# Optimization experiments

Measured on AMD Instinct MI355X. Metric: run time of the kernel, lower is better.

The kernel has to match this reference:

```python
import jax, jax.numpy as jnp
import numpy as np

DIM = 32  # fixed internal node dim
N_GRAPHS = 64


def setup_inputs() -> dict:
    key = jax.random.key(0)
    ks = jax.random.split(key, 16)
    N, E, F_N, F_E, H = 12500, 200000, 16, 8, 32
    inp = {
        "x": jax.random.normal(ks[0], (N, F_N), dtype=jnp.float32),
        "edge_index": jax.random.randint(ks[1], (2, E), 0, N, dtype=jnp.int64),
        "edge_attr": jax.random.normal(ks[2], (E, F_E), dtype=jnp.float32),
        "batch": jnp.sort(jax.random.randint(ks[3], (N,), 0, N_GRAPHS, dtype=jnp.int64)),
        "lin0_w": jax.random.normal(ks[4], (DIM, F_N), dtype=jnp.float32) * 0.1,
        "lin0_b": jax.random.normal(ks[5], (DIM,), dtype=jnp.float32) * 0.1,
        "nn_w": jax.random.normal(ks[6], (DIM * H, F_E), dtype=jnp.float32) * 0.1,
        "nn_b": jax.random.normal(ks[7], (DIM * H,), dtype=jnp.float32) * 0.1,
        "root_w": jax.random.normal(ks[8], (DIM, H), dtype=jnp.float32) * 0.1,
        "conv_b": jax.random.normal(ks[9], (H,), dtype=jnp.float32) * 0.1,
        "lin1_w": jax.random.normal(ks[10], (16, H), dtype=jnp.float32) * 0.1,
        "lin1_b": jax.random.normal(ks[11], (16,), dtype=jnp.float32) * 0.1,
        "lin2_w": jax.random.normal(ks[12], (1, 16), dtype=jnp.float32) * 0.1,
        "lin2_b": jax.random.normal(ks[13], (1,), dtype=jnp.float32) * 0.1,
    }
    return inp


def reference(x, edge_index, edge_attr, batch, lin0_w, lin0_b, nn_w, nn_b,
              root_w, conv_b, lin1_w, lin1_b, lin2_w, lin2_b):
    N = x.shape[0]
    H = conv_b.shape[0]
    # lin0 + relu -> node features [N, DIM]
    out = jax.nn.relu(x @ lin0_w.T + lin0_b)
    # NNConv: per-edge weight matrices from edge MLP (single Linear)
    src, dst = edge_index[0], edge_index[1]
    w_e = (edge_attr @ nn_w.T + nn_b).reshape(-1, DIM, H)  # [E, DIM, H]
    msg = jnp.einsum('ed,edh->eh', out[src], w_e)          # gather + per-edge matmul
    agg = jax.ops.segment_sum(msg, dst, num_segments=N)     # scatter-add
    h = jax.nn.relu(agg + out @ root_w + conv_b)             # root weight + bias
    # global add pool over graphs
    u = jax.ops.segment_sum(h, batch, num_segments=N_GRAPHS)  # [G, H]
    o = jax.nn.relu(u @ lin1_w.T + lin1_b)
    o = o @ lin2_w.T + lin2_b
    return o.reshape(-1)
```

## Files before the change

### kernel.cpp

```cpp
#include <hip/hip_runtime.h>

#define DIMN 32
#define HD   32
#define FN   16
#define FE   8
#define NG   64
#define CAP  64
#define K3T  512
#define K3W  (K3T / 64)

__global__ __launch_bounds__(256) void k1_out(
    const float* __restrict__ x, const float* __restrict__ lin0_w,
    const float* __restrict__ lin0_b,
    float* __restrict__ outn, float* __restrict__ aggfb, float* __restrict__ u,
    int* __restrict__ deg, int N)
{
    const int gt = blockIdx.x * 256 + threadIdx.x;
    if (gt >= N * DIMN) return;
    const int n = gt >> 5, d = gt & 31;

    float s = lin0_b[d];
    const float* xr = x + (size_t)n * FN;
    const float* wr = lin0_w + d * FN;
    #pragma unroll
    for (int j = 0; j < FN; ++j) s = fmaf(xr[j], wr[j], s);
    outn[gt] = fmaxf(s, 0.f);

    aggfb[gt] = 0.f;
    if (d == 0) deg[n] = 0;
    if (gt < NG * HD) u[gt] = 0.f;
}

__global__ __launch_bounds__(256) void kb_bucket(
    const int* __restrict__ ei, const float* __restrict__ ea,
    const float* __restrict__ outn, const float* __restrict__ nn_w,
    const float* __restrict__ nn_b,
    int* __restrict__ deg, int2* __restrict__ es, float* __restrict__ aggfb, int E)
{
    const int e = blockIdx.x * 256 + threadIdx.x;
    if (e >= E) return;
    const int src = ei[e];
    const int dst = ei[E + e];
    const int pos = atomicAdd(&deg[dst], 1);
    if (pos < CAP) {
        es[(size_t)dst * CAP + pos] = make_int2(e, src);
    } else {
        float ef[FE];
        #pragma unroll
        for (int f = 0; f < FE; ++f) ef[f] = ea[(size_t)e * FE + f];
        for (int h = 0; h < HD; ++h) {
            float m = 0.f;
            for (int d = 0; d < DIMN; ++d) {
                float wdh = nn_b[d * HD + h];
                #pragma unroll
                for (int f = 0; f < FE; ++f)
                    wdh = fmaf(ef[f], nn_w[(d * HD + h) * FE + f], wdh);
                m = fmaf(outn[(size_t)src * DIMN + d], wdh, m);
            }
            atomicAdd(aggfb + (size_t)dst * HD + h, m);
        }
    }
}

#define EDGE_FMA(o, a) \
    S  = (S + (o));                      \
    T0 = fmaf((o), (a).x, T0);           \
    T1 = fmaf((o), (a).y, T1);           \
    T2 = fmaf((o), (a).z, T2);           \
    T3 = fmaf((o), (a).w, T3);

#define CONTRIB(DD, A) { \
    const int d_ = d0 + (DD); \
    const float4 ta_ = *(const float4*)&s_T[w * 256 + d_ * 8]; \
    const float4 tb_ = *(const float4*)&s_T[w * 256 + d_ * 8 + 4]; \
    const float2 so_ = s_SO[w * 32 + d_]; \
    const int b_ = d_ * 256 + h; \
    A = fmaf(ta_.x, s_nnw2[b_      ], A); \
    A = fmaf(ta_.y, s_nnw2[b_ +  32], A); \
    A = fmaf(ta_.z, s_nnw2[b_ +  64], A); \
    A = fmaf(ta_.w, s_nnw2[b_ +  96], A); \
    A = fmaf(tb_.x, s_nnw2[b_ + 128], A); \
    A = fmaf(tb_.y, s_nnw2[b_ + 160], A); \
    A = fmaf(tb_.z, s_nnw2[b_ + 192], A); \
    A = fmaf(tb_.w, s_nnw2[b_ + 224], A); \
    A = fmaf(so_.x, s_nnb[d_ * 32 + h], A); \
    A = fmaf(so_.y, s_rw [d_ * 32 + h], A); }

__global__ __launch_bounds__(K3T, 8) void k3_gather(
    const float* __restrict__ ea, const float* __restrict__ outn,
    const int2* __restrict__ es, const float* __restrict__ nn_w,
    const float* __restrict__ nn_b, const float* __restrict__ root_w,
    const float* __restrict__ conv_b, const int* __restrict__ deg,
    const float* __restrict__ aggfb, const int* __restrict__ batch,
    float* __restrict__ u, int N)
{
    __shared__ float  s_nnw2[DIMN * FE * HD];
    __shared__ float  s_nnb[DIMN * HD];
    __shared__ float  s_rw[DIMN * HD];
    __shared__ float  s_cb[HD];
    __shared__ float  s_T[K3W * 256];
    __shared__ float2 s_SO[K3W * 32];
    __shared__ float  s_V[K3W * 32];
    __shared__ int    s_G[K3W];

    const int tid = threadIdx.x;
    for (int i = tid; i < DIMN * FE * HD; i += K3T) {
        const int d = i >> 8, rem = i & 255, hh = rem >> 3, f = rem & 7;
        s_nnw2[(d * 8 + f) * 32 + hh] = nn_w[i];
    }
    for (int i = tid; i < DIMN * HD; i += K3T) { s_nnb[i] = nn_b[i]; s_rw[i] = root_w[i]; }
    if (tid < HD) s_cb[tid] = conv_b[tid];
    __syncthreads();

    const int l = tid & 63;
    const int h = l & 31;
    const int p = l >> 5;
    const int w = tid >> 6;
    const int n = blockIdx.x * K3W + w;

    int gval = -1;
    if (n < N) {
        const int nu = __builtin_amdgcn_readfirstlane(n);
        const int dn = min(deg[nu], CAP);
        const int2* ep = es + (size_t)nu * CAP;
        const int f0 = 4 * p;

        float T0 = 0.f, T1 = 0.f, T2 = 0.f, T3 = 0.f, S = 0.f;

        for (int j0 = 0; j0 < dn; j0 += 8) {
            const int jm = dn - 1;
            const int2 E0 = ep[j0];
            const int2 E1 = ep[min(j0 + 1, jm)];
            const int2 E2 = ep[min(j0 + 2, jm)];
            const int2 E3 = ep[min(j0 + 3, jm)];
            const int2 E4 = ep[min(j0 + 4, jm)];
            const int2 E5 = ep[min(j0 + 5, jm)];
            const int2 E6 = ep[min(j0 + 6, jm)];
            const int2 E7 = ep[min(j0 + 7, jm)];

            const float4 a0 = *(const float4*)(ea + (size_t)E0.x * FE + f0);
            const float4 a1 = *(const float4*)(ea + (size_t)E1.x * FE + f0);
            const float4 a2 = *(const float4*)(ea + (size_t)E2.x * FE + f0);
            const float4 a3 = *(const float4*)(ea + (size_t)E3.x * FE + f0);
            const float4 a4 = *(const float4*)(ea + (size_t)E4.x * FE + f0);
            const float4 a5 = *(const float4*)(ea + (size_t)E5.x * FE + f0);
            const float4 a6 = *(const float4*)(ea + (size_t)E6.x * FE + f0);
            const float4 a7 = *(const float4*)(ea + (size_t)E7.x * FE + f0);
            float o0 = outn[(size_t)E0.y * DIMN + h];
            float o1 = outn[(size_t)E1.y * DIMN + h];
            float o2 = outn[(size_t)E2.y * DIMN + h];
            float o3 = outn[(size_t)E3.y * DIMN + h];
            float o4 = outn[(size_t)E4.y * DIMN + h];
            float o5 = outn[(size_t)E5.y * DIMN + h];
            float o6 = outn[(size_t)E6.y * DIMN + h];
            float o7 = outn[(size_t)E7.y * DIMN + h];

            o1 = (j0 + 1 <= jm) ? o1 : 0.f;
            o2 = (j0 + 2 <= jm) ? o2 : 0.f;
            o3 = (j0 + 3 <= jm) ? o3 : 0.f;
            o4 = (j0 + 4 <= jm) ? o4 : 0.f;
            o5 = (j0 + 5 <= jm) ? o5 : 0.f;
            o6 = (j0 + 6 <= jm) ? o6 : 0.f;
            o7 = (j0 + 7 <= jm) ? o7 : 0.f;

            EDGE_FMA(o0, a0) EDGE_FMA(o1, a1) EDGE_FMA(o2, a2) EDGE_FMA(o3, a3)
            EDGE_FMA(o4, a4) EDGE_FMA(o5, a5) EDGE_FMA(o6, a6) EDGE_FMA(o7, a7)
        }

        *(float4*)&s_T[w * 256 + h * 8 + f0] = make_float4(T0, T1, T2, T3);
        if (p == 0) s_SO[w * 32 + h] = make_float2(S, outn[(size_t)nu * DIMN + h]);

        const float base = aggfb[(size_t)nu * HD + h] + s_cb[h];

        float acc0 = 0.f, acc1 = 0.f, acc2 = 0.f, acc3 = 0.f;
        const int d0 = p << 4;
        #pragma unroll
        for (int dd = 0; dd < 16; dd += 4) {
            CONTRIB(dd + 0, acc0)
            CONTRIB(dd + 1, acc1)
            CONTRIB(dd + 2, acc2)
            CONTRIB(dd + 3, acc3)
        }
        float acc = (acc0 + acc1) + (acc2 + acc3);
        acc += __shfl_xor(acc, 32);

        const float v = fmaxf(acc + base, 0.f);
        if (p == 0) s_V[w * 32 + h] = v;
        gval = batch[nu];
    }
    if (l == 0) s_G[w] = gval;
    __syncthreads();

    if (tid < 32) {
        float accp = 0.f;
        int   gc   = -1;
        #pragma unroll
        for (int ww = 0; ww < K3W; ++ww) {
            const int gg = s_G[ww];
            if (gg >= 0) {
                const float vv = s_V[ww * 32 + tid];
                if (gg != gc) {
                    if (gc >= 0) atomicAdd(u + (size_t)gc * HD + tid, accp);
                    gc = gg;
                    accp = vv;
                } else {
                    accp += vv;
                }
            }
        }
        if (gc >= 0) atomicAdd(u + (size_t)gc * HD + tid, accp);
    }
}

__global__ __launch_bounds__(64) void k4_head(
    const float* __restrict__ u, const float* __restrict__ lin1_w,
    const float* __restrict__ lin1_b, const float* __restrict__ lin2_w,
    const float* __restrict__ lin2_b, float* __restrict__ outp)
{
    const int g = threadIdx.x;
    if (g >= NG) return;

    float ur[HD];
    #pragma unroll
    for (int hh = 0; hh < HD; ++hh) ur[hh] = u[(size_t)g * HD + hh];

    float acc = lin2_b[0];
    #pragma unroll
    for (int i = 0; i < 16; ++i) {
        float o = lin1_b[i];
        #pragma unroll
        for (int hh = 0; hh < HD; ++hh)
            o = fmaf(ur[hh], lin1_w[i * HD + hh], o);
        o = fmaxf(o, 0.f);
        acc = fmaf(o, lin2_w[i], acc);
    }
    outp[g] = acc;
}

extern "C" void kernel_launch(void* const* d_in, const int* in_sizes, int n_in,
                              void* d_out, int out_size, void* d_ws, size_t ws_size,
                              hipStream_t stream)
{
    const float* x      = (const float*)d_in[0];
    const int*   ei     = (const int*)  d_in[1];
    const float* ea     = (const float*)d_in[2];
    const int*   batch  = (const int*)  d_in[3];
    const float* lin0_w = (const float*)d_in[4];
    const float* lin0_b = (const float*)d_in[5];
    const float* nn_w   = (const float*)d_in[6];
    const float* nn_b   = (const float*)d_in[7];
    const float* root_w = (const float*)d_in[8];
    const float* conv_b = (const float*)d_in[9];
    const float* lin1_w = (const float*)d_in[10];
    const float* lin1_b = (const float*)d_in[11];
    const float* lin2_w = (const float*)d_in[12];
    const float* lin2_b = (const float*)d_in[13];

    const int N = in_sizes[0] / FN;
    const int E = in_sizes[2] / FE;

    float* ws    = (float*)d_ws;
    float* outn  = ws;
    float* aggfb = outn  + (size_t)N * DIMN;
    float* u     = aggfb + (size_t)N * DIMN;
    int*   deg   = (int*)(u + (size_t)NG * HD);
    int2*  es    = (int2*)(deg + N);

    const int nb1 = (N * DIMN + 255) / 256;
    k1_out<<<nb1, 256, 0, stream>>>(x, lin0_w, lin0_b, outn, aggfb, u, deg, N);

    const int nbb = (E + 255) / 256;
    kb_bucket<<<nbb, 256, 0, stream>>>(ei, ea, outn, nn_w, nn_b, deg, es, aggfb, E);

    const int nb3 = (N + K3W - 1) / K3W;
    k3_gather<<<nb3, K3T, 0, stream>>>(ea, outn, es, nn_w, nn_b, root_w, conv_b,
                                       deg, aggfb, batch, u, N);

    k4_head<<<1, 64, 0, stream>>>(u, lin1_w, lin1_b, lin2_w, lin2_b, (float*)d_out);
}
```

Baseline: 141.7 us.

## Process two destination nodes per wavefront in gather kernel with interleaved edge loops

Each wavefront in the gather kernel now handles two consecutive destination nodes. It interleaves their edge loads four edges at a time, so more independent gathers are in flight per iteration. The block count is halved and the occupancy hint is lowered from 8 to 6 to make room for the extra accumulator registers. The first bucket slot of every node is zero-initialised so clamped indices stay safe when a node has no edges. The trade-off is lower occupancy and wasted lanes whenever the two nodes' degrees differ.

```diff
diff --git a/kernel.cpp b/kernel.cpp
--- a/kernel.cpp
+++ b/kernel.cpp
@@ -8,12 +8,13 @@
 #define CAP  64
 #define K3T  512
 #define K3W  (K3T / 64)
+#define K3NPB (K3W * 2)
 
 __global__ __launch_bounds__(256) void k1_out(
     const float* __restrict__ x, const float* __restrict__ lin0_w,
     const float* __restrict__ lin0_b,
     float* __restrict__ outn, float* __restrict__ aggfb, float* __restrict__ u,
-    int* __restrict__ deg, int N)
+    int* __restrict__ deg, int2* __restrict__ es, int N)
 {
     const int gt = blockIdx.x * 256 + threadIdx.x;
     if (gt >= N * DIMN) return;
@@ -27,7 +28,7 @@
     outn[gt] = fmaxf(s, 0.f);
 
     aggfb[gt] = 0.f;
-    if (d == 0) deg[n] = 0;
+    if (d == 0) { deg[n] = 0; es[(size_t)n * CAP] = make_int2(0, 0); }
     if (gt < NG * HD) u[gt] = 0.f;
 }
 
@@ -62,12 +63,14 @@
     }
 }
 
-#define EDGE_FMA(o, a) \
-    S  = (S + (o));                      \
-    T0 = fmaf((o), (a).x, T0);           \
-    T1 = fmaf((o), (a).y, T1);           \
-    T2 = fmaf((o), (a).z, T2);           \
-    T3 = fmaf((o), (a).w, T3);
+#define EDGE_FMA_A(o, a) \
+    SA += (o); \
+    TA0 = fmaf((o), (a).x, TA0);  TA1 = fmaf((o), (a).y, TA1); \
+    TA2 = fmaf((o), (a).z, TA2);  TA3 = fmaf((o), (a).w, TA3);
+#define EDGE_FMA_B(o, a) \
+    SB += (o); \
+    TB0 = fmaf((o), (a).x, TB0);  TB1 = fmaf((o), (a).y, TB1); \
+    TB2 = fmaf((o), (a).z, TB2);  TB3 = fmaf((o), (a).w, TB3);
 
 #define CONTRIB(DD, A) { \
     const int d_ = d0 + (DD); \
@@ -86,7 +89,7 @@
     A = fmaf(so_.x, s_nnb[d_ * 32 + h], A); \
     A = fmaf(so_.y, s_rw [d_ * 32 + h], A); }
 
-__global__ __launch_bounds__(K3T, 8) void k3_gather(
+__global__ __launch_bounds__(K3T, 6) void k3_gather(
     const float* __restrict__ ea, const float* __restrict__ outn,
     const int2* __restrict__ es, const float* __restrict__ nn_w,
     const float* __restrict__ nn_b, const float* __restrict__ root_w,
@@ -100,8 +103,8 @@
     __shared__ float  s_cb[HD];
     __shared__ float  s_T[K3W * 256];
     __shared__ float2 s_SO[K3W * 32];
-    __shared__ float  s_V[K3W * 32];
-    __shared__ int    s_G[K3W];
+    __shared__ float  s_V[K3NPB * 32];
+    __shared__ int    s_G[K3NPB];
 
     const int tid = threadIdx.x;
     for (int i = tid; i < DIMN * FE * HD; i += K3T) {
@@ -116,86 +119,115 @@
     const int h = l & 31;
     const int p = l >> 5;
     const int w = tid >> 6;
-    const int n = blockIdx.x * K3W + w;
-
-    int gval = -1;
-    if (n < N) {
-        const int nu = __builtin_amdgcn_readfirstlane(n);
-        const int dn = min(deg[nu], CAP);
-        const int2* ep = es + (size_t)nu * CAP;
+    const int nA = blockIdx.x * K3NPB + 2 * w;
+
+    int gA = -1, gB = -1;
+    if (nA < N) {
+        const int nuA = __builtin_amdgcn_readfirstlane(nA);
+        const bool vB = (nuA + 1) < N;
+        const int nuB = vB ? nuA + 1 : nuA;
+        const int dnA = min(deg[nuA], CAP);
+        const int dnB = vB ? min(deg[nuB], CAP) : 0;
+        const int2* epA = es + (size_t)nuA * CAP;
+        const int2* epB = es + (size_t)nuB * CAP;
+        const int jmA = max(dnA - 1, 0);
+        const int jmB = max(dnB - 1, 0);
+        const int dmax = max(dnA, dnB);
         const int f0 = 4 * p;
 
-        float T0 = 0.f, T1 = 0.f, T2 = 0.f, T3 = 0.f, S = 0.f;
-
-        for (int j0 = 0; j0 < dn; j0 += 8) {
-            const int jm = dn - 1;
-            const int2 E0 = ep[j0];
-            const int2 E1 = ep[min(j0 + 1, jm)];
-            const int2 E2 = ep[min(j0 + 2, jm)];
-            const int2 E3 = ep[min(j0 + 3, jm)];
-            const int2 E4 = ep[min(j0 + 4, jm)];
-            const int2 E5 = ep[min(j0 + 5, jm)];
-            const int2 E6 = ep[min(j0 + 6, jm)];
-            const int2 E7 = ep[min(j0 + 7, jm)];
-
-            const float4 a0 = *(const float4*)(ea + (size_t)E0.x * FE + f0);
-            const float4 a1 = *(const float4*)(ea + (size_t)E1.x * FE + f0);
-            const float4 a2 = *(const float4*)(ea + (size_t)E2.x * FE + f0);
-            const float4 a3 = *(const float4*)(ea + (size_t)E3.x * FE + f0);
-            const float4 a4 = *(const float4*)(ea + (size_t)E4.x * FE + f0);
-            const float4 a5 = *(const float4*)(ea + (size_t)E5.x * FE + f0);
-            const float4 a6 = *(const float4*)(ea + (size_t)E6.x * FE + f0);
-            const float4 a7 = *(const float4*)(ea + (size_t)E7.x * FE + f0);
-            float o0 = outn[(size_t)E0.y * DIMN + h];
-            float o1 = outn[(size_t)E1.y * DIMN + h];
-            float o2 = outn[(size_t)E2.y * DIMN + h];
-            float o3 = outn[(size_t)E3.y * DIMN + h];
-            float o4 = outn[(size_t)E4.y * DIMN + h];
-            float o5 = outn[(size_t)E5.y * DIMN + h];
-            float o6 = outn[(size_t)E6.y * DIMN + h];
-            float o7 = outn[(size_t)E7.y * DIMN + h];
-
-            o1 = (j0 + 1 <= jm) ? o1 : 0.f;
-            o2 = (j0 + 2 <= jm) ? o2 : 0.f;
-            o3 = (j0 + 3 <= jm) ? o3 : 0.f;
-            o4 = (j0 + 4 <= jm) ? o4 : 0.f;
-            o5 = (j0 + 5 <= jm) ? o5 : 0.f;
-            o6 = (j0 + 6 <= jm) ? o6 : 0.f;
-            o7 = (j0 + 7 <= jm) ? o7 : 0.f;
-
-            EDGE_FMA(o0, a0) EDGE_FMA(o1, a1) EDGE_FMA(o2, a2) EDGE_FMA(o3, a3)
-            EDGE_FMA(o4, a4) EDGE_FMA(o5, a5) EDGE_FMA(o6, a6) EDGE_FMA(o7, a7)
-        }
-
-        *(float4*)&s_T[w * 256 + h * 8 + f0] = make_float4(T0, T1, T2, T3);
-        if (p == 0) s_SO[w * 32 + h] = make_float2(S, outn[(size_t)nu * DIMN + h]);
-
-        const float base = aggfb[(size_t)nu * HD + h] + s_cb[h];
-
-        float acc0 = 0.f, acc1 = 0.f, acc2 = 0.f, acc3 = 0.f;
+        float TA0 = 0.f, TA1 = 0.f, TA2 = 0.f, TA3 = 0.f, SA = 0.f;
+        float TB0 = 0.f, TB1 = 0.f, TB2 = 0.f, TB3 = 0.f, SB = 0.f;
+
+        for (int j0 = 0; j0 < dmax; j0 += 4) {
+            const int2 A0 = epA[min(j0 + 0, jmA)];
+            const int2 A1 = epA[min(j0 + 1, jmA)];
+            const int2 A2 = epA[min(j0 + 2, jmA)];
+            const int2 A3 = epA[min(j0 + 3, jmA)];
+            const int2 B0 = epB[min(j0 + 0, jmB)];
+            const int2 B1 = epB[min(j0 + 1, jmB)];
+            const int2 B2 = epB[min(j0 + 2, jmB)];
+            const int2 B3 = epB[min(j0 + 3, jmB)];
+
+            const float4 aA0 = *(const float4*)(ea + (size_t)A0.x * FE + f0);
+            const float4 aA1 = *(const float4*)(ea + (size_t)A1.x * FE + f0);
+            const float4 aA2 = *(const float4*)(ea + (size_t)A2.x * FE + f0);
+            const float4 aA3 = *(const float4*)(ea + (size_t)A3.x * FE + f0);
+            const float4 aB0 = *(const float4*)(ea + (size_t)B0.x * FE + f0);
+            const float4 aB1 = *(const float4*)(ea + (size_t)B1.x * FE + f0);
+            const float4 aB2 = *(const float4*)(ea + (size_t)B2.x * FE + f0);
+            const float4 aB3 = *(const float4*)(ea + (size_t)B3.x * FE + f0);
+            float oA0 = outn[(size_t)A0.y * DIMN + h];
+            float oA1 = outn[(size_t)A1.y * DIMN + h];
+            float oA2 = outn[(size_t)A2.y * DIMN + h];
+            float oA3 = outn[(size_t)A3.y * DIMN + h];
+            float oB0 = outn[(size_t)B0.y * DIMN + h];
+            float oB1 = outn[(size_t)B1.y * DIMN + h];
+            float oB2 = outn[(size_t)B2.y * DIMN + h];
+            float oB3 = outn[(size_t)B3.y * DIMN + h];
+
+            oA0 = (j0 + 0 < dnA) ? oA0 : 0.f;
+            oA1 = (j0 + 1 < dnA) ? oA1 : 0.f;
+            oA2 = (j0 + 2 < dnA) ? oA2 : 0.f;
+            oA3 = (j0 + 3 < dnA) ? oA3 : 0.f;
+            oB0 = (j0 + 0 < dnB) ? oB0 : 0.f;
+            oB1 = (j0 + 1 < dnB) ? oB1 : 0.f;
+            oB2 = (j0 + 2 < dnB) ? oB2 : 0.f;
+            oB3 = (j0 + 3 < dnB) ? oB3 : 0.f;
+
+            EDGE_FMA_A(oA0, aA0) EDGE_FMA_A(oA1, aA1)
+            EDGE_FMA_A(oA2, aA2) EDGE_FMA_A(oA3, aA3)
+            EDGE_FMA_B(oB0, aB0) EDGE_FMA_B(oB1, aB1)
+            EDGE_FMA_B(oB2, aB2) EDGE_FMA_B(oB3, aB3)
+        }
+
         const int d0 = p << 4;
-        #pragma unroll
-        for (int dd = 0; dd < 16; dd += 4) {
-            CONTRIB(dd + 0, acc0)
-            CONTRIB(dd + 1, acc1)
-            CONTRIB(dd + 2, acc2)
-            CONTRIB(dd + 3, acc3)
-        }
-        float acc = (acc0 + acc1) + (acc2 + acc3);
-        acc += __shfl_xor(acc, 32);
-
-        const float v = fmaxf(acc + base, 0.f);
-        if (p == 0) s_V[w * 32 + h] = v;
-        gval = batch[nu];
-    }
-    if (l == 0) s_G[w] = gval;
+
+        *(float4*)&s_T[w * 256 + h * 8 + f0] = make_float4(TA0, TA1, TA2, TA3);
+        if (p == 0) s_SO[w * 32 + h] = make_float2(SA, outn[(size_t)nuA * DIMN + h]);
+        {
+            const float base = aggfb[(size_t)nuA * HD + h] + s_cb[h];
+            float acc0 = 0.f, acc1 = 0.f, acc2 = 0.f, acc3 = 0.f;
+            #pragma unroll
+            for (int dd = 0; dd < 16; dd += 4) {
+                CONTRIB(dd + 0, acc0)
+                CONTRIB(dd + 1, acc1)
+                CONTRIB(dd + 2, acc2)
+                CONTRIB(dd + 3, acc3)
+            }
+            float acc = (acc0 + acc1) + (acc2 + acc3);
+            acc += __shfl_xor(acc, 32);
+            const float v = fmaxf(acc + base, 0.f);
+            if (p == 0) s_V[(2 * w) * 32 + h] = v;
+            gA = batch[nuA];
+        }
+
+        if (vB) {
+            *(float4*)&s_T[w * 256 + h * 8 + f0] = make_float4(TB0, TB1, TB2, TB3);
+            if (p == 0) s_SO[w * 32 + h] = make_float2(SB, outn[(size_t)nuB * DIMN + h]);
+            const float base = aggfb[(size_t)nuB * HD + h] + s_cb[h];
+            float acc0 = 0.f, acc1 = 0.f, acc2 = 0.f, acc3 = 0.f;
+            #pragma unroll
+            for (int dd = 0; dd < 16; dd += 4) {
+                CONTRIB(dd + 0, acc0)
+                CONTRIB(dd + 1, acc1)
+                CONTRIB(dd + 2, acc2)
+                CONTRIB(dd + 3, acc3)
+            }
+            float acc = (acc0 + acc1) + (acc2 + acc3);
+            acc += __shfl_xor(acc, 32);
+            const float v = fmaxf(acc + base, 0.f);
+            if (p == 0) s_V[(2 * w + 1) * 32 + h] = v;
+            gB = batch[nuB];
+        }
+    }
+    if (l == 0) { s_G[2 * w] = gA; s_G[2 * w + 1] = gB; }
     __syncthreads();
 
     if (tid < 32) {
         float accp = 0.f;
         int   gc   = -1;
         #pragma unroll
-        for (int ww = 0; ww < K3W; ++ww) {
+        for (int ww = 0; ww < K3NPB; ++ww) {
             const int gg = s_G[ww];
             if (gg >= 0) {
                 const float vv = s_V[ww * 32 + tid];
@@ -267,12 +299,12 @@
     int2*  es    = (int2*)(deg + N);
 
     const int nb1 = (N * DIMN + 255) / 256;
-    k1_out<<<nb1, 256, 0, stream>>>(x, lin0_w, lin0_b, outn, aggfb, u, deg, N);
+    k1_out<<<nb1, 256, 0, stream>>>(x, lin0_w, lin0_b, outn, aggfb, u, deg, es, N);
 
     const int nbb = (E + 255) / 256;
     kb_bucket<<<nbb, 256, 0, stream>>>(ei, ea, outn, nn_w, nn_b, deg, es, aggfb, E);
 
-    const int nb3 = (N + K3W - 1) / K3W;
+    const int nb3 = (N + K3NPB - 1) / K3NPB;
     k3_gather<<<nb3, K3T, 0, stream>>>(ea, outn, es, nn_w, nn_b, root_w, conv_b,
                                        deg, aggfb, batch, u, N);
 
```

New measurement: 148.2 us. +4.6%, slower.
